# Performance work log

Measured on AMD Instinct MI355X. Metric: run time of the kernel, lower is better.

## Reference

```python
import jax, jax.numpy as jnp
import numpy as np

E = 1024
H = 16
D = E // H
T = 1024
S = 1024
B = 8
MASK_FILL = 1e-30  # note: module fills masked scores with 1e-30, NOT -inf


def setup_inputs() -> dict:
    key = jax.random.key(0)
    ks = jax.random.split(key, 8)
    inp = {
        "query1": jax.random.normal(ks[0], (T, B, E), jnp.float32),
        "query2": jax.random.normal(ks[1], (T, B, E), jnp.float32),
        "key": jax.random.normal(ks[2], (S, B, E), jnp.float32),
        "value": jax.random.normal(ks[3], (S, B, E), jnp.float32),
        # causal mask: True = masked
        "attn_mask": jnp.triu(jnp.ones((T, S), jnp.bool_), k=1),
        # xavier-uniform-ish weights (torch stores Linear weight as [out, in])
        "q_w": jax.random.uniform(ks[4], (E, E), jnp.float32, -1, 1) * np.sqrt(6.0 / (2 * E)),
        "k_w": jax.random.uniform(ks[5], (E, E), jnp.float32, -1, 1) * np.sqrt(6.0 / (2 * E)),
        "v_w": jax.random.uniform(ks[6], (E, E), jnp.float32, -1, 1) * np.sqrt(6.0 / (2 * E)),
        "out_w": jax.random.uniform(ks[7], (E, E), jnp.float32, -1, 1) * np.sqrt(6.0 / (2 * E)),
    }
    return inp


def _split_heads(x):
    # [L, B, E] -> [B, H, L, D]
    L = x.shape[0]
    return x.reshape(L, B, H, D).transpose(1, 2, 0, 3)


def reference(query1, query2, key, value, attn_mask, q_w, k_w, v_w, out_w):
    scaling = float(D) ** -0.5
    q1 = _split_heads(query1 @ q_w.T) * scaling  # [B,H,T,D]
    q2 = _split_heads(query2 @ q_w.T) * scaling
    k = _split_heads(key @ k_w.T)                # [B,H,S,D]
    v = _split_heads(value @ v_w.T)

    # ---- stream s (second query stream attends first) ----
    scores_s = jnp.einsum("bhtd,bhsd->bhts", q2, k)
    scores_s = jnp.where(attn_mask[None, None], MASK_FILL, scores_s)
    probs_s = jax.nn.softmax(scores_s, axis=-1)
    o_s = jnp.einsum("bhts,bhsd->bhtd", probs_s, v)  # [B,H,T,D]

    # k/v update between passes (requires T == S)
    k2 = k + o_s
    v2 = v + o_s

    # ---- stream d ----
    scores_d = jnp.einsum("bhtd,bhsd->bhts", q1, k2)
    scores_d = jnp.where(attn_mask[None, None], MASK_FILL, scores_d)
    probs_d = jax.nn.softmax(scores_d, axis=-1)
    o_d = jnp.einsum("bhts,bhsd->bhtd", probs_d, v2)

    def _merge_and_proj(o):
        # [B,H,T,D] -> [T,B,E] -> out proj (no bias)
        return o.transpose(2, 0, 1, 3).reshape(T, B, E) @ out_w.T

    attn_output_s = _merge_and_proj(o_s)
    attn_output_d = _merge_and_proj(o_d)
    attn_s = probs_s.mean(axis=1)  # [B,T,S]
    attn_d = probs_d.mean(axis=1)
    return attn_output_d, attn_d, attn_output_s, attn_s
```

## Files before the change

kernel.cpp:

```cpp
#include <hip/hip_runtime.h>
#include <cstddef>

#define T_DIM 1024
#define S_DIM 1024
#define B_DIM 8
#define E_DIM 1024
#define H_DIM 16
#define D_DIM 64
#define NBHTD (B_DIM*H_DIM*T_DIM*D_DIM)

typedef __attribute__((ext_vector_type(8))) short short8;
typedef __attribute__((ext_vector_type(4))) short short4v;
typedef __attribute__((ext_vector_type(4))) float floatx4;

__device__ inline unsigned short f2bf(float x){
    union { float f; unsigned u; } v; v.f = x;
    unsigned r = (v.u + 0x7FFFu + ((v.u >> 16) & 1u)) >> 16;
    return (unsigned short)r;
}
__device__ inline float bf2f(unsigned short h){
    union { float f; unsigned u; } v; v.u = ((unsigned)h) << 16; return v.f;
}

typedef __attribute__((address_space(1))) const unsigned int* gptr_t;
typedef __attribute__((address_space(3))) unsigned int* lptr_t;
__device__ inline void gl_lds16(const void* g, void* l){
    __builtin_amdgcn_global_load_lds((gptr_t)g, (lptr_t)l, 16, 0, 0);
}

__device__ inline int poff(int row, int s){
    return (row << 10) + ((((s >> 3) ^ (row & 7)) << 3)) + (s & 7);
}

__global__ __launch_bounds__(256)
void split_pair(const float* __restrict__ src, unsigned short* __restrict__ hi,
                unsigned short* __restrict__ lo, float scale)
{
    size_t i = ((size_t)blockIdx.x*256 + threadIdx.x)*8;
    float4 a = *(const float4*)(src+i);
    float4 b = *(const float4*)(src+i+4);
    float v[8] = {a.x,a.y,a.z,a.w,b.x,b.y,b.z,b.w};
    short8 h8, l8;
    #pragma unroll
    for (int j = 0; j < 8; ++j) {
        float x = v[j]*scale;
        unsigned short hh = f2bf(x);
        h8[j] = (short)hh;
        l8[j] = (short)f2bf(x - bf2f(hh));
    }
    *(short8*)(hi+i) = h8;
    *(short8*)(lo+i) = l8;
}

template <int AMODE, int CMODE>
__global__ __launch_bounds__(256, 2)
void gemm_bf3(const unsigned short* __restrict__ Ahi, const unsigned short* __restrict__ Alo,
              const unsigned short* __restrict__ Bhi, const unsigned short* __restrict__ Blo,
              float* __restrict__ Cf,
              unsigned short* __restrict__ Chi, unsigned short* __restrict__ Clo)
{
    __shared__ __align__(16) unsigned short lds[4][128*32];

    const int tid  = threadIdx.x;
    const int n0   = blockIdx.x * 128;
    const int m0   = blockIdx.y * 128;
    const int wave = tid >> 6, lane = tid & 63;
    const int lrow = lane & 15, quad = lane >> 4;
    const int mw = (wave & 1)*64, nw = (wave >> 1)*64;

    floatx4 acc[4][4];
    #pragma unroll
    for (int i = 0; i < 4; ++i)
        #pragma unroll
        for (int j = 0; j < 4; ++j) acc[i][j] = (floatx4){0.f,0.f,0.f,0.f};

    for (int kk = 0; kk < 1024; kk += 32) {
        __syncthreads();
        #pragma unroll
        for (int rnd = 0; rnd < 2; ++rnd) {
            int c = rnd*256 + tid;
            int row = c >> 2, col8 = (c & 3)*8;
            size_t aoff;
            if (AMODE == 0) {
                aoff = (size_t)(m0+row)*1024 + kk + col8;
            } else {
                int r = m0 + row; int t = r >> 3, bb = r & 7;
                int h = kk >> 6, d0 = (kk & 63) + col8;
                aoff = (((size_t)(bb*H_DIM + h)*T_DIM) + t)*D_DIM + d0;
            }
            size_t boff = (size_t)(n0+row)*1024 + kk + col8;
            gl_lds16(Ahi + aoff, &lds[0][c*8]);
            gl_lds16(Alo + aoff, &lds[1][c*8]);
            gl_lds16(Bhi + boff, &lds[2][c*8]);
            gl_lds16(Blo + boff, &lds[3][c*8]);
        }
        __syncthreads();

        short8 ah[4], al[4], bh[4], bl[4];
        #pragma unroll
        for (int mt = 0; mt < 4; ++mt) {
            int r = mw + mt*16 + lrow;
            ah[mt] = *(const short8*)&lds[0][r*32 + quad*8];
            al[mt] = *(const short8*)&lds[1][r*32 + quad*8];
        }
        #pragma unroll
        for (int nt = 0; nt < 4; ++nt) {
            int r = nw + nt*16 + lrow;
            bh[nt] = *(const short8*)&lds[2][r*32 + quad*8];
            bl[nt] = *(const short8*)&lds[3][r*32 + quad*8];
        }
        #pragma unroll
        for (int mt = 0; mt < 4; ++mt)
            #pragma unroll
            for (int nt = 0; nt < 4; ++nt) {
                acc[mt][nt] = __builtin_amdgcn_mfma_f32_16x16x32_bf16(ah[mt], bh[nt], acc[mt][nt], 0,0,0);
                acc[mt][nt] = __builtin_amdgcn_mfma_f32_16x16x32_bf16(ah[mt], bl[nt], acc[mt][nt], 0,0,0);
                acc[mt][nt] = __builtin_amdgcn_mfma_f32_16x16x32_bf16(al[mt], bh[nt], acc[mt][nt], 0,0,0);
            }
    }

    #pragma unroll
    for (int mt = 0; mt < 4; ++mt) {
        #pragma unroll
        for (int nt = 0; nt < 4; ++nt) {
            int n = n0 + nw + nt*16 + lrow;
            #pragma unroll
            for (int r = 0; r < 4; ++r) {
                int m = m0 + mw + mt*16 + quad*4 + r;
                float v = acc[mt][nt][r];
                if (CMODE == 2) {
                    Cf[(size_t)m*1024 + n] = v;
                } else {
                    int t = m >> 3, bb = m & 7;
                    int h = n >> 6, d = n & 63;
                    size_t idx = (((size_t)(bb*H_DIM + h)*T_DIM) + t)*D_DIM + d;
                    if (CMODE == 0) {
                        Cf[idx] = v;
                    } else {
                        unsigned short hh = f2bf(v);
                        Chi[idx] = hh;
                        Clo[idx] = f2bf(v - bf2f(hh));
                    }
                }
            }
        }
    }
}

__global__ __launch_bounds__(256)
void split_vt(const float* __restrict__ Vh, unsigned short* __restrict__ Vthi,
              unsigned short* __restrict__ Vtlo)
{
    __shared__ float tile[64][68];
    const int bh = blockIdx.y, s0 = blockIdx.x*64;
    const int tid = threadIdx.x;
    const size_t base = (size_t)bh*S_DIM*D_DIM;

    {
        int r = tid >> 2, c0 = (tid & 3) * 16;
        const float* p = Vh + base + (size_t)(s0 + r)*D_DIM + c0;
        float4 a = *(const float4*)p;
        float4 b = *(const float4*)(p+4);
        float4 c = *(const float4*)(p+8);
        float4 d = *(const float4*)(p+12);
        *(float4*)&tile[r][c0]    = a;
        *(float4*)&tile[r][c0+4]  = b;
        *(float4*)&tile[r][c0+8]  = c;
        *(float4*)&tile[r][c0+12] = d;
    }
    __syncthreads();
    {
        int d = tid >> 2, cs = (tid & 3) * 16;
        short8 hi[2], lo[2];
        #pragma unroll
        for (int half = 0; half < 2; ++half)
            #pragma unroll
            for (int u = 0; u < 8; ++u) {
                float x = tile[cs + half*8 + u][d];
                unsigned short hh = f2bf(x);
                hi[half][u] = (short)hh;
                lo[half][u] = (short)f2bf(x - bf2f(hh));
            }
        size_t obase = base + (size_t)d*S_DIM + s0 + cs;
        *(short8*)(Vthi + obase)     = hi[0];
        *(short8*)(Vthi + obase + 8) = hi[1];
        *(short8*)(Vtlo + obase)     = lo[0];
        *(short8*)(Vtlo + obase + 8) = lo[1];
    }
}

__global__ __launch_bounds__(512, 2)
void attn_mfma(const float* __restrict__ Qh,
               const unsigned short* __restrict__ Khi, const unsigned short* __restrict__ Klo,
               const unsigned short* __restrict__ Vthi, const unsigned short* __restrict__ Vtlo,
               float* __restrict__ Ofp,
               unsigned short* __restrict__ Ohi, unsigned short* __restrict__ Olo,
               float* __restrict__ attn_mean)
{
    const int bid = blockIdx.x;
    const int b   = bid & 7;
    const int t0  = (bid >> 3) * 16;
    const int tid  = threadIdx.x;
    const int lane = tid & 63;
    const int wave = tid >> 6;
    const int lrow = lane & 15;
    const int quad = lane >> 4;
    const int t_g  = t0 + lrow;

    __shared__ __align__(16) unsigned short plds[16*1024];
    __shared__ float2 stats[8][16];
    __shared__ float  pbuf[4][16][16];

    float accm[32];
    #pragma unroll
    for (int i = 0; i < 32; ++i) accm[i] = 0.f;

    #pragma unroll 1
    for (int h = 0; h < H_DIM; ++h) {
        const int bh = b*H_DIM + h;
        const size_t kbase = (size_t)bh * S_DIM * D_DIM;

        short8 qh0, ql0, qh1, ql1;
        {
            const float* qp = Qh + kbase + (size_t)(t0 + lrow)*D_DIM + quad*8;
            float4 a  = *(const float4*)qp;
            float4 b4 = *(const float4*)(qp+4);
            float4 c4 = *(const float4*)(qp+32);
            float4 d4 = *(const float4*)(qp+36);
            float va[8]  = {a.x,a.y,a.z,a.w,b4.x,b4.y,b4.z,b4.w};
            float vb8[8] = {c4.x,c4.y,c4.z,c4.w,d4.x,d4.y,d4.z,d4.w};
            #pragma unroll
            for (int j = 0; j < 8; ++j) {
                unsigned short h0 = f2bf(va[j]);
                qh0[j] = (short)h0; ql0[j] = (short)f2bf(va[j] - bf2f(h0));
                unsigned short h1 = f2bf(vb8[j]);
                qh1[j] = (short)h1; ql1[j] = (short)f2bf(vb8[j] - bf2f(h1));
            }
        }

        float sv[32];
        {
            const unsigned short* kph = Khi + kbase + (size_t)(wave*128 + lrow)*D_DIM + quad*8;
            const unsigned short* kpl = Klo + kbase + (size_t)(wave*128 + lrow)*D_DIM + quad*8;
            short8 kh0 = *(const short8*)(kph);
            short8 kh1 = *(const short8*)(kph + 32);
            short8 kl0 = *(const short8*)(kpl);
            short8 kl1 = *(const short8*)(kpl + 32);
            #pragma unroll
            for (int jt = 0; jt < 8; ++jt) {
                short8 nh0, nh1, nl0, nl1;
                if (jt < 7) {
                    const unsigned short* nph = kph + (jt+1)*16*D_DIM;
                    const unsigned short* npl = kpl + (jt+1)*16*D_DIM;
                    nh0 = *(const short8*)(nph);
                    nh1 = *(const short8*)(nph + 32);
                    nl0 = *(const short8*)(npl);
                    nl1 = *(const short8*)(npl + 32);
                }
                floatx4 acc = {0.f,0.f,0.f,0.f};
                acc = __builtin_amdgcn_mfma_f32_16x16x32_bf16(kh0, qh0, acc, 0,0,0);
                acc = __builtin_amdgcn_mfma_f32_16x16x32_bf16(kh1, qh1, acc, 0,0,0);
                acc = __builtin_amdgcn_mfma_f32_16x16x32_bf16(kl0, qh0, acc, 0,0,0);
                acc = __builtin_amdgcn_mfma_f32_16x16x32_bf16(kl1, qh1, acc, 0,0,0);
                acc = __builtin_amdgcn_mfma_f32_16x16x32_bf16(kh0, ql0, acc, 0,0,0);
                acc = __builtin_amdgcn_mfma_f32_16x16x32_bf16(kh1, ql1, acc, 0,0,0);
                const int sb = wave*128 + jt*16 + quad*4;
                #pragma unroll
                for (int r = 0; r < 4; ++r)
                    sv[jt*4+r] = (sb + r > t_g) ? 1e-30f : acc[r];
                kh0 = nh0; kh1 = nh1; kl0 = nl0; kl1 = nl1;
            }
        }

        float mt[16];
        #pragma unroll
        for (int i = 0; i < 16; ++i) mt[i] = fmaxf(sv[i], sv[i+16]);
        #pragma unroll
        for (int st = 8; st > 0; st >>= 1) {
            #pragma unroll
            for (int i = 0; i < st; ++i) mt[i] = fmaxf(mt[i], mt[i+st]);
        }
        float m_loc = fmaxf(mt[0], __shfl_xor(mt[0], 16));
        m_loc = fmaxf(m_loc, __shfl_xor(m_loc, 32));

        #pragma unroll
        for (int i = 0; i < 32; ++i) sv[i] = __expf(sv[i] - m_loc);
        float st2[16];
        #pragma unroll
        for (int i = 0; i < 16; ++i) st2[i] = sv[i] + sv[i+16];
        #pragma unroll
        for (int st = 8; st > 0; st >>= 1) {
            #pragma unroll
            for (int i = 0; i < st; ++i) st2[i] += st2[i+st];
        }
        float s_loc = st2[0] + __shfl_xor(st2[0], 16);
        s_loc += __shfl_xor(s_loc, 32);

        if (quad == 0) stats[wave][lrow] = make_float2(m_loc, s_loc);
        __syncthreads();

        float m_g, sum_g;
        {
            float2 c0 = stats[0][lrow], c1 = stats[1][lrow];
            float2 c2 = stats[2][lrow], c3 = stats[3][lrow];
            float2 c4 = stats[4][lrow], c5 = stats[5][lrow];
            float2 c6 = stats[6][lrow], c7 = stats[7][lrow];
            m_g = fmaxf(fmaxf(fmaxf(c0.x, c1.x), fmaxf(c2.x, c3.x)),
                        fmaxf(fmaxf(c4.x, c5.x), fmaxf(c6.x, c7.x)));
            sum_g = c0.y*__expf(c0.x - m_g) + c1.y*__expf(c1.x - m_g)
                  + c2.y*__expf(c2.x - m_g) + c3.y*__expf(c3.x - m_g)
                  + c4.y*__expf(c4.x - m_g) + c5.y*__expf(c5.x - m_g)
                  + c6.y*__expf(c6.x - m_g) + c7.y*__expf(c7.x - m_g);
        }
        const float myscale = __expf(m_loc - m_g) / sum_g;

        #pragma unroll
        for (int jt = 0; jt < 8; ++jt) {
            float p0 = sv[jt*4+0]*myscale, p1 = sv[jt*4+1]*myscale;
            float p2 = sv[jt*4+2]*myscale, p3 = sv[jt*4+3]*myscale;
            accm[jt*4+0] += p0; accm[jt*4+1] += p1;
            accm[jt*4+2] += p2; accm[jt*4+3] += p3;
            short4v pk;
            pk[0] = (short)f2bf(p0); pk[1] = (short)f2bf(p1);
            pk[2] = (short)f2bf(p2); pk[3] = (short)f2bf(p3);
            const int sidx = wave*128 + jt*16 + quad*4;
            *(short4v*)&plds[poff(lrow, sidx)] = pk;
        }
        __syncthreads();

        {
            const int d0    = (wave & 3)*16;
            const int shalf = (wave >> 2)*512;
            const unsigned short* vh = Vthi + kbase + (size_t)(d0 + lrow)*S_DIM;
            const unsigned short* vl = Vtlo + kbase + (size_t)(d0 + lrow)*S_DIM;
            floatx4 oa = {0.f,0.f,0.f,0.f}, ob = {0.f,0.f,0.f,0.f};
            #pragma unroll 4
            for (int sk = 0; sk < 512; sk += 32) {
                const int sa = shalf + sk + quad*8;
                short8 af  = *(const short8*)&plds[poff(lrow, sa)];
                short8 bh8 = *(const short8*)(vh + sa);
                short8 bl8 = *(const short8*)(vl + sa);
                oa = __builtin_amdgcn_mfma_f32_16x16x32_bf16(af, bh8, oa, 0,0,0);
                ob = __builtin_amdgcn_mfma_f32_16x16x32_bf16(af, bl8, ob, 0,0,0);
            }
            if (wave >= 4) {
                #pragma unroll
                for (int r = 0; r < 4; ++r)
                    pbuf[wave-4][quad*4+r][lrow] = oa[r] + ob[r];
            }
            __syncthreads();
            if (wave < 4) {
                #pragma unroll
                for (int r = 0; r < 4; ++r) {
                    int q = quad*4 + r;
                    float v = oa[r] + ob[r] + pbuf[wave][q][lrow];
                    size_t idx = kbase + (size_t)(t0+q)*D_DIM + d0 + lrow;
                    if (Ofp) Ofp[idx] = v;
                    unsigned short hh = f2bf(v);
                    Ohi[idx] = hh;
                    Olo[idx] = f2bf(v - bf2f(hh));
                }
            }
        }
    }

    {
        float* am = attn_mean + ((size_t)b*T_DIM + t_g)*S_DIM + wave*128 + quad*4;
        #pragma unroll
        for (int jt = 0; jt < 8; ++jt) {
            float4 p4;
            p4.x = accm[jt*4+0]*(1.0f/H_DIM);
            p4.y = accm[jt*4+1]*(1.0f/H_DIM);
            p4.z = accm[jt*4+2]*(1.0f/H_DIM);
            p4.w = accm[jt*4+3]*(1.0f/H_DIM);
            *(float4*)(am + jt*16) = p4;
        }
    }
}

__global__ __launch_bounds__(256)
void add_k(unsigned short* __restrict__ Khi, unsigned short* __restrict__ Klo,
           const float* __restrict__ O)
{
    size_t i = ((size_t)blockIdx.x*256 + threadIdx.x)*8;
    short8 hi = *(short8*)(Khi+i), lo = *(short8*)(Klo+i);
    float4 o0 = *(const float4*)(O+i), o1 = *(const float4*)(O+i+4);
    float ov[8] = {o0.x,o0.y,o0.z,o0.w,o1.x,o1.y,o1.z,o1.w};
    short8 nh, nl;
    #pragma unroll
    for (int j = 0; j < 8; ++j) {
        float k = bf2f((unsigned short)hi[j]) + bf2f((unsigned short)lo[j]) + ov[j];
        unsigned short hh = f2bf(k);
        nh[j] = (short)hh;
        nl[j] = (short)f2bf(k - bf2f(hh));
    }
    *(short8*)(Khi+i) = nh;
    *(short8*)(Klo+i) = nl;
}

__global__ __launch_bounds__(256)
void add_v(float* __restrict__ V, const float* __restrict__ O)
{
    size_t i = ((size_t)blockIdx.x*256 + threadIdx.x)*4;
    float4 o = *(const float4*)(O+i);
    float4 v = *(const float4*)(V+i);
    v.x+=o.x; v.y+=o.y; v.z+=o.z; v.w+=o.w;
    *(float4*)(V+i) = v;
}

extern "C" void kernel_launch(void* const* d_in, const int* in_sizes, int n_in,
                              void* d_out, int out_size, void* d_ws, size_t ws_size,
                              hipStream_t stream)
{
    const float* q1  = (const float*)d_in[0];
    const float* q2  = (const float*)d_in[1];
    const float* key = (const float*)d_in[2];
    const float* val = (const float*)d_in[3];
    const float* qw  = (const float*)d_in[5];
    const float* kw  = (const float*)d_in[6];
    const float* vw  = (const float*)d_in[7];
    const float* ow  = (const float*)d_in[8];

    float* out   = (float*)d_out;
    float* outd  = out;
    float* attnd = out + 1*(size_t)NBHTD;
    float* outs  = out + 2*(size_t)NBHTD;
    float* attns = out + 3*(size_t)NBHTD;

    unsigned short* ws_u16 = (unsigned short*)d_ws;
    unsigned short* Khi  = ws_u16;
    unsigned short* Klo  = Khi  + (size_t)NBHTD;
    unsigned short* Vthi = Klo  + (size_t)NBHTD;
    unsigned short* Vtlo = Vthi + (size_t)NBHTD;
    unsigned short* R2a  = Vtlo + (size_t)NBHTD;
    unsigned short* R2b  = R2a  + 2*(size_t)NBHTD;

    const size_t EE = (size_t)E_DIM*E_DIM;
    unsigned short* qwhi = R2a;
    unsigned short* qwlo = qwhi + EE;
    unsigned short* kwhi = qwlo + EE;
    unsigned short* kwlo = kwhi + EE;
    unsigned short* vwhi = kwlo + EE;
    unsigned short* vwlo = vwhi + EE;
    float* Osb = (float*)R2a;
    unsigned short* Odhi = R2a;
    unsigned short* Odlo = Odhi + (size_t)NBHTD;
    unsigned short* Oshi = R2b;
    unsigned short* Oslo = Oshi + (size_t)NBHTD;
    unsigned short* owhi = ws_u16;
    unsigned short* owlo = owhi + EE;

    float* Q1h = outd;
    float* Q2h = outs;
    float* Vh  = attnd;
    unsigned short* Ahi = (unsigned short*)attns;
    unsigned short* Alo = Ahi + (size_t)NBHTD;

    const dim3 ggrid(8, 64);

    split_pair<<<512, 256, 0, stream>>>(qw, qwhi, qwlo, 1.f);
    split_pair<<<512, 256, 0, stream>>>(kw, kwhi, kwlo, 1.f);
    split_pair<<<512, 256, 0, stream>>>(vw, vwhi, vwlo, 1.f);

    split_pair<<<4096, 256, 0, stream>>>(key, Ahi, Alo, 1.f);
    gemm_bf3<0,1><<<ggrid, 256, 0, stream>>>(Ahi, Alo, kwhi, kwlo, nullptr, Khi, Klo);

    split_pair<<<4096, 256, 0, stream>>>(val, Ahi, Alo, 1.f);
    gemm_bf3<0,0><<<ggrid, 256, 0, stream>>>(Ahi, Alo, vwhi, vwlo, Vh, nullptr, nullptr);
    split_vt<<<dim3(16, 128), 256, 0, stream>>>(Vh, Vthi, Vtlo);

    split_pair<<<4096, 256, 0, stream>>>(q1, Ahi, Alo, 0.125f);
    gemm_bf3<0,0><<<ggrid, 256, 0, stream>>>(Ahi, Alo, qwhi, qwlo, Q1h, nullptr, nullptr);

    split_pair<<<4096, 256, 0, stream>>>(q2, Ahi, Alo, 0.125f);
    gemm_bf3<0,0><<<ggrid, 256, 0, stream>>>(Ahi, Alo, qwhi, qwlo, Q2h, nullptr, nullptr);

    attn_mfma<<<dim3(512), 512, 0, stream>>>(Q2h, Khi, Klo, Vthi, Vtlo,
                                             Osb, Oshi, Oslo, attns);

    add_k<<<4096, 256, 0, stream>>>(Khi, Klo, Osb);
    add_v<<<8192, 256, 0, stream>>>(Vh, Osb);
    split_vt<<<dim3(16, 128), 256, 0, stream>>>(Vh, Vthi, Vtlo);

    attn_mfma<<<dim3(512), 512, 0, stream>>>(Q1h, Khi, Klo, Vthi, Vtlo,
                                             nullptr, Odhi, Odlo, attnd);

    split_pair<<<512, 256, 0, stream>>>(ow, owhi, owlo, 1.f);
    gemm_bf3<1,2><<<ggrid, 256, 0, stream>>>(Oshi, Oslo, owhi, owlo, outs, nullptr, nullptr);
    gemm_bf3<1,2><<<ggrid, 256, 0, stream>>>(Odhi, Odlo, owhi, owlo, outd, nullptr, nullptr);
}
```

Before: 1.724 ms.

## Split attention heads across two blocks and drop softmax max pass

Each attention block now handles only half the heads, doubling the grid, and writes a partial head-sum of the probabilities. A new merge kernel adds the two partials and applies the 1/H scaling. The softmax drops max subtraction and exponentiates raw scores in the QK loop, relying on scores staying small enough not to overflow. The fp32 O buffer write is removed, so the K/V update kernels rebuild O from its hi/lo bf16 pair, and launch bounds allow four blocks per CU. The extra merge passes add memory traffic, and softmax without max subtraction is numerically unsafe for large scores.

After: 1.738 ms. No clear change (+0.8%).

```diff
diff --git a/kernel.cpp b/kernel.cpp
--- a/kernel.cpp
+++ b/kernel.cpp
@@ -189,17 +189,17 @@
     }
 }
 
-__global__ __launch_bounds__(512, 2)
+__global__ __launch_bounds__(512, 4)
 void attn_mfma(const float* __restrict__ Qh,
                const unsigned short* __restrict__ Khi, const unsigned short* __restrict__ Klo,
                const unsigned short* __restrict__ Vthi, const unsigned short* __restrict__ Vtlo,
-               float* __restrict__ Ofp,
                unsigned short* __restrict__ Ohi, unsigned short* __restrict__ Olo,
-               float* __restrict__ attn_mean)
+               float* __restrict__ mean0, float* __restrict__ mean1)
 {
     const int bid = blockIdx.x;
     const int b   = bid & 7;
-    const int t0  = (bid >> 3) * 16;
+    const int t0  = ((bid >> 3) & 63) * 16;
+    const int hh  = bid >> 9;
     const int tid  = threadIdx.x;
     const int lane = tid & 63;
     const int wave = tid >> 6;
@@ -208,7 +208,7 @@
     const int t_g  = t0 + lrow;
 
     __shared__ __align__(16) unsigned short plds[16*1024];
-    __shared__ float2 stats[8][16];
+    __shared__ float  stats[8][16];
     __shared__ float  pbuf[4][16][16];
 
     float accm[32];
@@ -216,7 +216,7 @@
     for (int i = 0; i < 32; ++i) accm[i] = 0.f;
 
     #pragma unroll 1
-    for (int h = 0; h < H_DIM; ++h) {
+    for (int h = hh*8; h < hh*8 + 8; ++h) {
         const int bh = b*H_DIM + h;
         const size_t kbase = (size_t)bh * S_DIM * D_DIM;
 
@@ -239,6 +239,7 @@
         }
 
         float sv[32];
+        float sum_loc = 0.f;
         {
             const unsigned short* kph = Khi + kbase + (size_t)(wave*128 + lrow)*D_DIM + quad*8;
             const unsigned short* kpl = Klo + kbase + (size_t)(wave*128 + lrow)*D_DIM + quad*8;
@@ -266,58 +267,29 @@
                 acc = __builtin_amdgcn_mfma_f32_16x16x32_bf16(kh1, ql1, acc, 0,0,0);
                 const int sb = wave*128 + jt*16 + quad*4;
                 #pragma unroll
-                for (int r = 0; r < 4; ++r)
-                    sv[jt*4+r] = (sb + r > t_g) ? 1e-30f : acc[r];
+                for (int r = 0; r < 4; ++r) {
+                    float sval = (sb + r > t_g) ? 1e-30f : acc[r];
+                    float p = __expf(sval);
+                    sv[jt*4+r] = p;
+                    sum_loc += p;
+                }
                 kh0 = nh0; kh1 = nh1; kl0 = nl0; kl1 = nl1;
             }
         }
 
-        float mt[16];
-        #pragma unroll
-        for (int i = 0; i < 16; ++i) mt[i] = fmaxf(sv[i], sv[i+16]);
-        #pragma unroll
-        for (int st = 8; st > 0; st >>= 1) {
-            #pragma unroll
-            for (int i = 0; i < st; ++i) mt[i] = fmaxf(mt[i], mt[i+st]);
-        }
-        float m_loc = fmaxf(mt[0], __shfl_xor(mt[0], 16));
-        m_loc = fmaxf(m_loc, __shfl_xor(m_loc, 32));
-
-        #pragma unroll
-        for (int i = 0; i < 32; ++i) sv[i] = __expf(sv[i] - m_loc);
-        float st2[16];
-        #pragma unroll
-        for (int i = 0; i < 16; ++i) st2[i] = sv[i] + sv[i+16];
-        #pragma unroll
-        for (int st = 8; st > 0; st >>= 1) {
-            #pragma unroll
-            for (int i = 0; i < st; ++i) st2[i] += st2[i+st];
-        }
-        float s_loc = st2[0] + __shfl_xor(st2[0], 16);
-        s_loc += __shfl_xor(s_loc, 32);
-
-        if (quad == 0) stats[wave][lrow] = make_float2(m_loc, s_loc);
+        sum_loc += __shfl_xor(sum_loc, 16);
+        sum_loc += __shfl_xor(sum_loc, 32);
+        if (quad == 0) stats[wave][lrow] = sum_loc;
         __syncthreads();
 
-        float m_g, sum_g;
-        {
-            float2 c0 = stats[0][lrow], c1 = stats[1][lrow];
-            float2 c2 = stats[2][lrow], c3 = stats[3][lrow];
-            float2 c4 = stats[4][lrow], c5 = stats[5][lrow];
-            float2 c6 = stats[6][lrow], c7 = stats[7][lrow];
-            m_g = fmaxf(fmaxf(fmaxf(c0.x, c1.x), fmaxf(c2.x, c3.x)),
-                        fmaxf(fmaxf(c4.x, c5.x), fmaxf(c6.x, c7.x)));
-            sum_g = c0.y*__expf(c0.x - m_g) + c1.y*__expf(c1.x - m_g)
-                  + c2.y*__expf(c2.x - m_g) + c3.y*__expf(c3.x - m_g)
-                  + c4.y*__expf(c4.x - m_g) + c5.y*__expf(c5.x - m_g)
-                  + c6.y*__expf(c6.x - m_g) + c7.y*__expf(c7.x - m_g);
-        }
-        const float myscale = __expf(m_loc - m_g) / sum_g;
+        float sum_g = ((stats[0][lrow] + stats[1][lrow]) + (stats[2][lrow] + stats[3][lrow]))
+                    + ((stats[4][lrow] + stats[5][lrow]) + (stats[6][lrow] + stats[7][lrow]));
+        const float inv = 1.0f / sum_g;
 
         #pragma unroll
         for (int jt = 0; jt < 8; ++jt) {
-            float p0 = sv[jt*4+0]*myscale, p1 = sv[jt*4+1]*myscale;
-            float p2 = sv[jt*4+2]*myscale, p3 = sv[jt*4+3]*myscale;
+            float p0 = sv[jt*4+0]*inv, p1 = sv[jt*4+1]*inv;
+            float p2 = sv[jt*4+2]*inv, p3 = sv[jt*4+3]*inv;
             accm[jt*4+0] += p0; accm[jt*4+1] += p1;
             accm[jt*4+2] += p2; accm[jt*4+3] += p3;
             short4v pk;
@@ -355,57 +327,75 @@
                     int q = quad*4 + r;
                     float v = oa[r] + ob[r] + pbuf[wave][q][lrow];
                     size_t idx = kbase + (size_t)(t0+q)*D_DIM + d0 + lrow;
-                    if (Ofp) Ofp[idx] = v;
-                    unsigned short hh = f2bf(v);
-                    Ohi[idx] = hh;
-                    Olo[idx] = f2bf(v - bf2f(hh));
+                    unsigned short hv = f2bf(v);
+                    Ohi[idx] = hv;
+                    Olo[idx] = f2bf(v - bf2f(hv));
                 }
             }
         }
     }
 
     {
-        float* am = attn_mean + ((size_t)b*T_DIM + t_g)*S_DIM + wave*128 + quad*4;
+        float* mp = (hh ? mean1 : mean0)
+                  + ((size_t)b*T_DIM + t_g)*S_DIM + wave*128 + quad*4;
         #pragma unroll
         for (int jt = 0; jt < 8; ++jt) {
             float4 p4;
-            p4.x = accm[jt*4+0]*(1.0f/H_DIM);
-            p4.y = accm[jt*4+1]*(1.0f/H_DIM);
-            p4.z = accm[jt*4+2]*(1.0f/H_DIM);
-            p4.w = accm[jt*4+3]*(1.0f/H_DIM);
-            *(float4*)(am + jt*16) = p4;
-        }
-    }
+            p4.x = accm[jt*4+0];
+            p4.y = accm[jt*4+1];
+            p4.z = accm[jt*4+2];
+            p4.w = accm[jt*4+3];
+            *(float4*)(mp + jt*16) = p4;
+        }
+    }
+}
+
+__global__ __launch_bounds__(256)
+void merge_mean(float* __restrict__ dst, const float* __restrict__ part)
+{
+    size_t i = ((size_t)blockIdx.x*256 + threadIdx.x)*4;
+    float4 a = *(const float4*)(dst+i);
+    float4 b = *(const float4*)(part+i);
+    a.x = (a.x+b.x)*0.0625f; a.y = (a.y+b.y)*0.0625f;
+    a.z = (a.z+b.z)*0.0625f; a.w = (a.w+b.w)*0.0625f;
+    *(float4*)(dst+i) = a;
 }
 
 __global__ __launch_bounds__(256)
 void add_k(unsigned short* __restrict__ Khi, unsigned short* __restrict__ Klo,
-           const float* __restrict__ O)
+           const unsigned short* __restrict__ Ohi, const unsigned short* __restrict__ Olo)
 {
     size_t i = ((size_t)blockIdx.x*256 + threadIdx.x)*8;
     short8 hi = *(short8*)(Khi+i), lo = *(short8*)(Klo+i);
-    float4 o0 = *(const float4*)(O+i), o1 = *(const float4*)(O+i+4);
-    float ov[8] = {o0.x,o0.y,o0.z,o0.w,o1.x,o1.y,o1.z,o1.w};
+    short8 oh = *(const short8*)(Ohi+i), ol = *(const short8*)(Olo+i);
     short8 nh, nl;
     #pragma unroll
     for (int j = 0; j < 8; ++j) {
-        float k = bf2f((unsigned short)hi[j]) + bf2f((unsigned short)lo[j]) + ov[j];
-        unsigned short hh = f2bf(k);
-        nh[j] = (short)hh;
-        nl[j] = (short)f2bf(k - bf2f(hh));
+        float o = bf2f((unsigned short)oh[j]) + bf2f((unsigned short)ol[j]);
+        float k = bf2f((unsigned short)hi[j]) + bf2f((unsigned short)lo[j]) + o;
+        unsigned short hv = f2bf(k);
+        nh[j] = (short)hv;
+        nl[j] = (short)f2bf(k - bf2f(hv));
     }
     *(short8*)(Khi+i) = nh;
     *(short8*)(Klo+i) = nl;
 }
 
 __global__ __launch_bounds__(256)
-void add_v(float* __restrict__ V, const float* __restrict__ O)
-{
-    size_t i = ((size_t)blockIdx.x*256 + threadIdx.x)*4;
-    float4 o = *(const float4*)(O+i);
-    float4 v = *(const float4*)(V+i);
-    v.x+=o.x; v.y+=o.y; v.z+=o.z; v.w+=o.w;
-    *(float4*)(V+i) = v;
+void add_v(float* __restrict__ V,
+           const unsigned short* __restrict__ Ohi, const unsigned short* __restrict__ Olo)
+{
+    size_t i = ((size_t)blockIdx.x*256 + threadIdx.x)*8;
+    short8 oh = *(const short8*)(Ohi+i), ol = *(const short8*)(Olo+i);
+    float4 v0 = *(const float4*)(V+i), v1 = *(const float4*)(V+i+4);
+    float v[8] = {v0.x,v0.y,v0.z,v0.w,v1.x,v1.y,v1.z,v1.w};
+    #pragma unroll
+    for (int j = 0; j < 8; ++j)
+        v[j] += bf2f((unsigned short)oh[j]) + bf2f((unsigned short)ol[j]);
+    v0.x=v[0]; v0.y=v[1]; v0.z=v[2]; v0.w=v[3];
+    v1.x=v[4]; v1.y=v[5]; v1.z=v[6]; v1.w=v[7];
+    *(float4*)(V+i)   = v0;
+    *(float4*)(V+i+4) = v1;
 }
 
 extern "C" void kernel_launch(void* const* d_in, const int* in_sizes, int n_in,
@@ -442,7 +432,7 @@
     unsigned short* kwlo = kwhi + EE;
     unsigned short* vwhi = kwlo + EE;
     unsigned short* vwlo = vwhi + EE;
-    float* Osb = (float*)R2a;
+    float* Ms1f = (float*)R2a;
     unsigned short* Odhi = R2a;
     unsigned short* Odlo = Odhi + (size_t)NBHTD;
     unsigned short* Oshi = R2b;
@@ -475,15 +465,17 @@
     split_pair<<<4096, 256, 0, stream>>>(q2, Ahi, Alo, 0.125f);
     gemm_bf3<0,0><<<ggrid, 256, 0, stream>>>(Ahi, Alo, qwhi, qwlo, Q2h, nullptr, nullptr);
 
-    attn_mfma<<<dim3(512), 512, 0, stream>>>(Q2h, Khi, Klo, Vthi, Vtlo,
-                                             Osb, Oshi, Oslo, attns);
-
-    add_k<<<4096, 256, 0, stream>>>(Khi, Klo, Osb);
-    add_v<<<8192, 256, 0, stream>>>(Vh, Osb);
+    attn_mfma<<<dim3(1024), 512, 0, stream>>>(Q2h, Khi, Klo, Vthi, Vtlo,
+                                              Oshi, Oslo, attns, Ms1f);
+    merge_mean<<<8192, 256, 0, stream>>>(attns, Ms1f);
+
+    add_k<<<4096, 256, 0, stream>>>(Khi, Klo, Oshi, Oslo);
+    add_v<<<4096, 256, 0, stream>>>(Vh, Oshi, Oslo);
     split_vt<<<dim3(16, 128), 256, 0, stream>>>(Vh, Vthi, Vtlo);
 
-    attn_mfma<<<dim3(512), 512, 0, stream>>>(Q1h, Khi, Klo, Vthi, Vtlo,
-                                             nullptr, Odhi, Odlo, attnd);
+    attn_mfma<<<dim3(1024), 512, 0, stream>>>(Q1h, Khi, Klo, Vthi, Vtlo,
+                                              Odhi, Odlo, attnd, outs);
+    merge_mean<<<8192, 256, 0, stream>>>(attnd, outs);
 
     split_pair<<<512, 256, 0, stream>>>(ow, owhi, owlo, 1.f);
     gemm_bf3<1,2><<<ggrid, 256, 0, stream>>>(Oshi, Oslo, owhi, owlo, outs, nullptr, nullptr);
```
